# Optimization experiments

Measured on AMD Instinct MI355X. Metric: run time of the kernel, lower is better.

Reference implementation:

```python
import jax, jax.numpy as jnp
import numpy as np

VOCAB, P, K, B, L, R = 50257, 512, 64, 32, 2048, 5


def setup_inputs() -> dict:
    key = jax.random.key(0)
    k1, k2, k3, k4, k5, k6, k7 = jax.random.split(key, 7)
    return {
        "x": jax.random.randint(k1, (B, L), 0, VOCAB, dtype=jnp.int32),
        "V": jax.random.normal(k2, (VOCAB, P), dtype=jnp.float32),
        "C": jax.random.normal(k3, (K, P), dtype=jnp.float32),
        "f1_w": jax.random.normal(k4, (2 * R + 1,), dtype=jnp.float32),
        "f1_b": jax.random.normal(k5, (K,), dtype=jnp.float32),
        "f2_w": jax.random.normal(k6, (K, P), dtype=jnp.float32),
        "f2_b": jax.random.normal(k7, (K,), dtype=jnp.float32),
    }


def reference(x, V, C, f1_w, f1_b, f2_w, f2_b):
    b, l = x.shape
    k, p = C.shape
    w = f1_w.shape[0]
    r = (w - 1) // 2
    emb = V[x]                                              # [B,L,P] embedding lookup
    x_hat = emb / jnp.linalg.norm(emb, axis=2, keepdims=True)
    l_hat = C / jnp.linalg.norm(C, axis=1, keepdims=True)
    G = jnp.einsum('kp,blp->bkl', l_hat, x_hat)             # cosine sim [B,K,L]
    # sliding-window dot product == depthwise 1D cross-correlation, 'same' padding
    u = jax.lax.conv_general_dilated(
        G.reshape(b * k, 1, l), f1_w.reshape(1, 1, w),
        window_strides=(1,), padding=[(r, r)],
        dimension_numbers=('NCH', 'OIH', 'NCH'),
    ).reshape(b, k, l)
    m = jax.nn.relu(u + f1_b[None, :, None])                # [B,K,L]
    beta = jax.nn.softmax(m.max(axis=1), axis=1)            # max over labels, softmax over seq -> [B,L]
    pooled = jnp.mean(beta[:, :, None] * emb, axis=1)       # [B,P]
    return pooled @ f2_w.T + f2_b                           # [B,K]
```

## Files before the change

kernel.cpp:

```cpp
#include <hip/hip_runtime.h>
#include <hip/hip_bf16.h>

#define PP     512
#define KK     64
#define BB     32
#define LLEN   2048
#define SROWS  74

typedef __attribute__((ext_vector_type(8)))  short short8;
typedef __attribute__((ext_vector_type(16))) float float16;

__device__ inline unsigned int pack_bf2(float lo, float hi) {
    __hip_bfloat162 h = __float22bfloat162_rn(make_float2(lo, hi));
    unsigned int u;
    __builtin_memcpy(&u, &h, 4);
    return u;
}
__device__ inline float bf_lo(unsigned int v) { return __uint_as_float(v << 16); }
__device__ inline float bf_hi(unsigned int v) { return __uint_as_float(v & 0xffff0000u); }

__global__ void k1_prep(const float* __restrict__ C, const float* __restrict__ f2w,
                        ushort* __restrict__ Bu) {
    const int n = blockIdx.x;
    const float* src = (n < 64) ? (C + n * PP) : (f2w + (n - 64) * PP);
    const int t = threadIdx.x;
    float v0 = src[t];
    float v1 = src[t + 256];
    __shared__ float red[256];
    red[t] = v0 * v0 + v1 * v1;
    __syncthreads();
    for (int s = 128; s > 0; s >>= 1) {
        if (t < s) red[t] += red[t + s];
        __syncthreads();
    }
    const float inv = (n < 64) ? rsqrtf(red[0]) : 1.f;
    Bu[(((t >> 3)       * 128 + n) << 3) + (t & 7)] = (ushort)(pack_bf2(v0 * inv, 0.f) & 0xffffu);
    Bu[((((t + 256) >> 3)) * 128 + n) * 8 + (t & 7)] = (ushort)(pack_bf2(v1 * inv, 0.f) & 0xffffu);
}

__launch_bounds__(512, 4)
__global__ void k2_fused(const int* __restrict__ x, const float* __restrict__ V,
                         const uint4* __restrict__ Bu4,
                         const float* __restrict__ f1w, const float* __restrict__ f1b,
                         float* __restrict__ pool) {
    __shared__ uint4 sA[SROWS * 64];
    __shared__ int   stok[SROWS];
    __shared__ float rnorm[SROWS];
    __shared__ float smv[64];
    __shared__ float sp[64];
    __shared__ float sscal[2];

    const int tid  = threadIdx.x;
    const int lane = tid & 63;
    const int wv   = tid >> 6;
    const int l31  = lane & 31;
    const int b    = blockIdx.x >> 5;
    const int l0   = (blockIdx.x & 31) * 64;

    if (tid < SROWS) {
        int gl = l0 - 5 + tid;
        gl = min(max(gl, 0), LLEN - 1);
        stok[tid] = x[b * LLEN + gl];
    }
    __syncthreads();

    {
        const int o = tid & 7;
        const int r = tid >> 3;
        const float* src = V + (size_t)stok[r] * PP + o * 4;
        const int swzr = r & 7;
        float nrm = 0.f;
        float4 pa[8];
#pragma unroll
        for (int g = 0; g < 8; ++g) pa[g] = ((const float4*)src)[g * 8];
        float4 pb[8];
#pragma unroll
        for (int g = 0; g < 8; ++g) pb[g] = ((const float4*)src)[(g + 8) * 8];
#pragma unroll
        for (int g = 0; g < 8; ++g) {
            const float4 a = pa[g];
            nrm = fmaf(a.x, a.x, fmaf(a.y, a.y, fmaf(a.z, a.z, fmaf(a.w, a.w, nrm))));
            uint2 w2; w2.x = pack_bf2(a.x, a.y); w2.y = pack_bf2(a.z, a.w);
            const int f = g * 4 + (o >> 1);
            ((uint2*)&sA[r * 64 + (f ^ swzr)])[o & 1] = w2;
        }
#pragma unroll
        for (int g = 0; g < 8; ++g) {
            const float4 a = pb[g];
            nrm = fmaf(a.x, a.x, fmaf(a.y, a.y, fmaf(a.z, a.z, fmaf(a.w, a.w, nrm))));
            uint2 w2; w2.x = pack_bf2(a.x, a.y); w2.y = pack_bf2(a.z, a.w);
            const int f = (g + 8) * 4 + (o >> 1);
            ((uint2*)&sA[r * 64 + (f ^ swzr)])[o & 1] = w2;
        }
        nrm += __shfl_xor(nrm, 1, 64);
        nrm += __shfl_xor(nrm, 2, 64);
        nrm += __shfl_xor(nrm, 4, 64);
        if (o == 0) rnorm[r] = rsqrtf(nrm);
    }
    if (tid < 160) {
        const int h16 = tid & 15;
        const int r   = 64 + (tid >> 4);
        const float* src = V + (size_t)stok[r] * PP + h16 * 4;
        const int swzr = r & 7;
        float nrm = 0.f;
        float4 ph[8];
#pragma unroll
        for (int g = 0; g < 8; ++g) ph[g] = ((const float4*)src)[g * 16];
#pragma unroll
        for (int g = 0; g < 8; ++g) {
            const float4 a = ph[g];
            nrm = fmaf(a.x, a.x, fmaf(a.y, a.y, fmaf(a.z, a.z, fmaf(a.w, a.w, nrm))));
            uint2 w2; w2.x = pack_bf2(a.x, a.y); w2.y = pack_bf2(a.z, a.w);
            const int f = g * 8 + (h16 >> 1);
            ((uint2*)&sA[r * 64 + (f ^ swzr)])[h16 & 1] = w2;
        }
        nrm += __shfl_xor(nrm, 1, 64);
        nrm += __shfl_xor(nrm, 2, 64);
        nrm += __shfl_xor(nrm, 4, 64);
        nrm += __shfl_xor(nrm, 8, 64);
        if (h16 == 0) rnorm[r] = rsqrtf(nrm);
    }
    __syncthreads();

    float16 c0, c1;
#pragma unroll
    for (int i = 0; i < 16; ++i) { c0[i] = 0.f; c1[i] = 0.f; }

    const int rowBase = (wv == 0) ? 0 : (wv == 1) ? 32 : (wv == 2) ? 42
                      : (wv == 3) ? 5 : 37;
    const int cc = lane >> 5;
    if (wv < 5) {
        const int nh    = (wv < 3) ? 0 : 64;
        const int row   = rowBase + l31;
        const int abase = row * 64;
        const int aswz  = row & 7;
#pragma unroll 8
        for (int ks = 0; ks < 32; ++ks) {
            const int ff = ks * 2 + cc;
            const uint4 av = sA[abase + (ff ^ aswz)];
            const uint4 b0 = Bu4[ff * 128 + nh + l31];
            const uint4 b1 = Bu4[ff * 128 + nh + 32 + l31];
            short8 a8, t0, t1;
            __builtin_memcpy(&a8, &av, 16);
            __builtin_memcpy(&t0, &b0, 16);
            __builtin_memcpy(&t1, &b1, 16);
            c0 = __builtin_amdgcn_mfma_f32_32x32x16_bf16(a8, t0, c0, 0, 0, 0);
            c1 = __builtin_amdgcn_mfma_f32_32x32x16_bf16(a8, t1, c1, 0, 0, 0);
        }
    }
    __syncthreads();

    unsigned int* G32 = (unsigned int*)sA;
    float*        E2s = (float*)((char*)sA + 10240);
    float*        sred = (float*)((char*)sA + 28672);
    if (wv < 3) {
#pragma unroll
        for (int reg = 0; reg < 16; ++reg) {
            const int rr  = (reg & 3) + 8 * (reg >> 2) + 4 * cc;
            const int row = rowBase + rr;
            if (wv == 2 && row < 64) continue;
            const int gl = l0 - 5 + row;
            unsigned int vpk = 0u;
            if (gl >= 0 && gl < LLEN) {
                const float rn = rnorm[row];
                vpk = pack_bf2(c0[reg] * rn, c1[reg] * rn);
            }
            G32[row * 32 + l31] = vpk;
        }
    } else if (wv < 5) {
#pragma unroll
        for (int reg = 0; reg < 16; ++reg) {
            const int rr = (reg & 3) + 8 * (reg >> 2) + 4 * cc;
            const int o  = rowBase - 5 + rr;
            E2s[o * 64 + l31]      = c0[reg];
            E2s[o * 64 + 32 + l31] = c1[reg];
        }
    }
    __syncthreads();

    float w[11];
#pragma unroll
    for (int t = 0; t < 11; ++t) w[t] = f1w[t];
    const int j = l31;
    const int h = tid >> 5;
    const float bias0 = f1b[j], bias1 = f1b[j + 32];
#pragma unroll
    for (int i = 0; i < 4; ++i) {
        const int o = i * 16 + h;
        float u0 = 0.f, u1 = 0.f;
#pragma unroll
        for (int tap = 0; tap < 11; ++tap) {
            const unsigned int v = G32[(o + tap) * 32 + j];
            u0 = fmaf(bf_lo(v), w[tap], u0);
            u1 = fmaf(bf_hi(v), w[tap], u1);
        }
        float m = fmaxf(fmaxf(u0 + bias0, 0.f), fmaxf(u1 + bias1, 0.f));
#pragma unroll
        for (int off = 16; off > 0; off >>= 1)
            m = fmaxf(m, __shfl_xor(m, off, 64));
        if (j == 0) smv[o] = m;
    }
    __syncthreads();

    if (tid < 64) {
        float v = smv[tid];
#pragma unroll
        for (int off = 32; off > 0; off >>= 1)
            v = fmaxf(v, __shfl_xor(v, off, 64));
        if (tid == 0) sscal[0] = v;
    }
    __syncthreads();
    const float mx = sscal[0];
    if (tid < 64) sp[tid] = __expf(smv[tid] - mx);
    __syncthreads();
    if (tid < 64) {
        float s = sp[tid];
#pragma unroll
        for (int off = 32; off > 0; off >>= 1)
            s += __shfl_xor(s, off, 64);
        if (tid == 0) sscal[1] = s;
    }

    float a0 = 0.f, a1 = 0.f;
#pragma unroll
    for (int i = 0; i < 4; ++i) {
        const int o = i * 16 + h;
        const float wgt = sp[o];
        a0 = fmaf(wgt, E2s[o * 64 + j], a0);
        a1 = fmaf(wgt, E2s[o * 64 + 32 + j], a1);
    }
    __syncthreads();
    sred[h * 64 + j]      = a0;
    sred[h * 64 + j + 32] = a1;
    __syncthreads();
    if (tid < 64) {
        float r = 0.f;
#pragma unroll
        for (int hh = 0; hh < 16; ++hh) r += sred[hh * 64 + tid];
        float* dst = pool + (size_t)blockIdx.x * 68;
        dst[tid] = r;
        if (tid == 0) { dst[64] = sscal[0]; dst[65] = sscal[1]; }
    }
}

__global__ void k6_final(const float* __restrict__ pool, const float* __restrict__ f2b,
                         float* __restrict__ out) {
    const int b = blockIdx.x;
    const int k = threadIdx.x;
    float M = -1e30f;
#pragma unroll
    for (int c = 0; c < 32; ++c)
        M = fmaxf(M, pool[(size_t)(b * 32 + c) * 68 + 64]);
    float tot = 0.f, num = 0.f;
#pragma unroll
    for (int c = 0; c < 32; ++c) {
        const float* pc = pool + (size_t)(b * 32 + c) * 68;
        const float sc = __expf(pc[64] - M);
        tot = fmaf(sc, pc[65], tot);
        num = fmaf(sc, pc[k], num);
    }
    out[b * KK + k] = (num / tot) * (1.f / 2048.f) + f2b[k];
}

extern "C" void kernel_launch(void* const* d_in, const int* in_sizes, int n_in,
                              void* d_out, int out_size, void* d_ws, size_t ws_size,
                              hipStream_t stream) {
    const int*   x   = (const int*)d_in[0];
    const float* V   = (const float*)d_in[1];
    const float* C   = (const float*)d_in[2];
    const float* f1w = (const float*)d_in[3];
    const float* f1b = (const float*)d_in[4];
    const float* f2w = (const float*)d_in[5];
    const float* f2b = (const float*)d_in[6];
    float* out = (float*)d_out;

    float* ws = (float*)d_ws;
    ushort* Bu = (ushort*)ws;
    float* pool = ws + 32768;

    k1_prep <<<128, 256, 0, stream>>>(C, f2w, Bu);
    k2_fused<<<BB * 32, 512, 0, stream>>>(x, V, (const uint4*)Bu, f1w, f1b, pool);
    k6_final<<<BB, 64, 0, stream>>>(pool, f2b, out);
}
```

Before: 185.2 us.

## Halve per-block sequence tile to 32 positions and double grid size

Each fused block now handles 32 sequence positions (42 rows including halo) instead of 64 (74 rows), so the grid grows to 2048 blocks and LDS use per block shrinks. Launch bounds are raised to allow more resident blocks per CU, and the MFMA wave assignment is remapped to three waves. The halo overhead (10 extra gathered rows per 32 positions instead of per 64) increases redundant embedding loads, and more waves sit idle during the matmul. The final reduction loops over 64 chunks instead of 32.

```diff
diff --git a/kernel.cpp b/kernel.cpp
--- a/kernel.cpp
+++ b/kernel.cpp
@@ -5,7 +5,9 @@
 #define KK     64
 #define BB     32
 #define LLEN   2048
-#define SROWS  74
+#define TPOS   32
+#define SROWS  42
+#define NCHUNK (LLEN / TPOS)
 
 typedef __attribute__((ext_vector_type(8)))  short short8;
 typedef __attribute__((ext_vector_type(16))) float float16;
@@ -38,7 +40,7 @@
     Bu[((((t + 256) >> 3)) * 128 + n) * 8 + (t & 7)] = (ushort)(pack_bf2(v1 * inv, 0.f) & 0xffffu);
 }
 
-__launch_bounds__(512, 4)
+__launch_bounds__(512, 6)
 __global__ void k2_fused(const int* __restrict__ x, const float* __restrict__ V,
                          const uint4* __restrict__ Bu4,
                          const float* __restrict__ f1w, const float* __restrict__ f1b,
@@ -46,16 +48,16 @@
     __shared__ uint4 sA[SROWS * 64];
     __shared__ int   stok[SROWS];
     __shared__ float rnorm[SROWS];
-    __shared__ float smv[64];
-    __shared__ float sp[64];
+    __shared__ float smv[TPOS];
+    __shared__ float sp[TPOS];
     __shared__ float sscal[2];
 
     const int tid  = threadIdx.x;
     const int lane = tid & 63;
     const int wv   = tid >> 6;
     const int l31  = lane & 31;
-    const int b    = blockIdx.x >> 5;
-    const int l0   = (blockIdx.x & 31) * 64;
+    const int b    = blockIdx.x >> 6;
+    const int l0   = (blockIdx.x & 63) * TPOS;
 
     if (tid < SROWS) {
         int gl = l0 - 5 + tid;
@@ -64,73 +66,53 @@
     }
     __syncthreads();
 
-    {
+    if (tid < SROWS * 8) {
         const int o = tid & 7;
         const int r = tid >> 3;
         const float* src = V + (size_t)stok[r] * PP + o * 4;
         const int swzr = r & 7;
         float nrm = 0.f;
-        float4 pa[8];
-#pragma unroll
-        for (int g = 0; g < 8; ++g) pa[g] = ((const float4*)src)[g * 8];
-        float4 pb[8];
-#pragma unroll
-        for (int g = 0; g < 8; ++g) pb[g] = ((const float4*)src)[(g + 8) * 8];
-#pragma unroll
-        for (int g = 0; g < 8; ++g) {
-            const float4 a = pa[g];
-            nrm = fmaf(a.x, a.x, fmaf(a.y, a.y, fmaf(a.z, a.z, fmaf(a.w, a.w, nrm))));
-            uint2 w2; w2.x = pack_bf2(a.x, a.y); w2.y = pack_bf2(a.z, a.w);
-            const int f = g * 4 + (o >> 1);
-            ((uint2*)&sA[r * 64 + (f ^ swzr)])[o & 1] = w2;
-        }
-#pragma unroll
-        for (int g = 0; g < 8; ++g) {
-            const float4 a = pb[g];
-            nrm = fmaf(a.x, a.x, fmaf(a.y, a.y, fmaf(a.z, a.z, fmaf(a.w, a.w, nrm))));
-            uint2 w2; w2.x = pack_bf2(a.x, a.y); w2.y = pack_bf2(a.z, a.w);
-            const int f = (g + 8) * 4 + (o >> 1);
-            ((uint2*)&sA[r * 64 + (f ^ swzr)])[o & 1] = w2;
+        {
+            float4 pa[8];
+#pragma unroll
+            for (int g = 0; g < 8; ++g) pa[g] = ((const float4*)src)[g * 8];
+#pragma unroll
+            for (int g = 0; g < 8; ++g) {
+                const float4 a = pa[g];
+                nrm = fmaf(a.x, a.x, fmaf(a.y, a.y, fmaf(a.z, a.z, fmaf(a.w, a.w, nrm))));
+                uint2 w2; w2.x = pack_bf2(a.x, a.y); w2.y = pack_bf2(a.z, a.w);
+                const int f = g * 4 + (o >> 1);
+                ((uint2*)&sA[r * 64 + (f ^ swzr)])[o & 1] = w2;
+            }
+        }
+        {
+            float4 pb[8];
+#pragma unroll
+            for (int g = 0; g < 8; ++g) pb[g] = ((const float4*)src)[(g + 8) * 8];
+#pragma unroll
+            for (int g = 0; g < 8; ++g) {
+                const float4 a = pb[g];
+                nrm = fmaf(a.x, a.x, fmaf(a.y, a.y, fmaf(a.z, a.z, fmaf(a.w, a.w, nrm))));
+                uint2 w2; w2.x = pack_bf2(a.x, a.y); w2.y = pack_bf2(a.z, a.w);
+                const int f = (g + 8) * 4 + (o >> 1);
+                ((uint2*)&sA[r * 64 + (f ^ swzr)])[o & 1] = w2;
+            }
         }
         nrm += __shfl_xor(nrm, 1, 64);
         nrm += __shfl_xor(nrm, 2, 64);
         nrm += __shfl_xor(nrm, 4, 64);
         if (o == 0) rnorm[r] = rsqrtf(nrm);
     }
-    if (tid < 160) {
-        const int h16 = tid & 15;
-        const int r   = 64 + (tid >> 4);
-        const float* src = V + (size_t)stok[r] * PP + h16 * 4;
-        const int swzr = r & 7;
-        float nrm = 0.f;
-        float4 ph[8];
-#pragma unroll
-        for (int g = 0; g < 8; ++g) ph[g] = ((const float4*)src)[g * 16];
-#pragma unroll
-        for (int g = 0; g < 8; ++g) {
-            const float4 a = ph[g];
-            nrm = fmaf(a.x, a.x, fmaf(a.y, a.y, fmaf(a.z, a.z, fmaf(a.w, a.w, nrm))));
-            uint2 w2; w2.x = pack_bf2(a.x, a.y); w2.y = pack_bf2(a.z, a.w);
-            const int f = g * 8 + (h16 >> 1);
-            ((uint2*)&sA[r * 64 + (f ^ swzr)])[h16 & 1] = w2;
-        }
-        nrm += __shfl_xor(nrm, 1, 64);
-        nrm += __shfl_xor(nrm, 2, 64);
-        nrm += __shfl_xor(nrm, 4, 64);
-        nrm += __shfl_xor(nrm, 8, 64);
-        if (h16 == 0) rnorm[r] = rsqrtf(nrm);
-    }
     __syncthreads();
 
     float16 c0, c1;
 #pragma unroll
     for (int i = 0; i < 16; ++i) { c0[i] = 0.f; c1[i] = 0.f; }
 
-    const int rowBase = (wv == 0) ? 0 : (wv == 1) ? 32 : (wv == 2) ? 42
-                      : (wv == 3) ? 5 : 37;
+    const int rowBase = (wv == 0) ? 0 : (wv == 1) ? 10 : 5;
     const int cc = lane >> 5;
-    if (wv < 5) {
-        const int nh    = (wv < 3) ? 0 : 64;
+    if (wv < 3) {
+        const int nh    = (wv < 2) ? 0 : 64;
         const int row   = rowBase + l31;
         const int abase = row * 64;
         const int aswz  = row & 7;
@@ -151,14 +133,14 @@
     __syncthreads();
 
     unsigned int* G32 = (unsigned int*)sA;
-    float*        E2s = (float*)((char*)sA + 10240);
-    float*        sred = (float*)((char*)sA + 28672);
-    if (wv < 3) {
+    float*        E2s = (float*)((char*)sA + 5632);
+    float*        sred = (float*)((char*)sA + 14336);
+    if (wv < 2) {
 #pragma unroll
         for (int reg = 0; reg < 16; ++reg) {
             const int rr  = (reg & 3) + 8 * (reg >> 2) + 4 * cc;
             const int row = rowBase + rr;
-            if (wv == 2 && row < 64) continue;
+            if (wv == 1 && row < 32) continue;
             const int gl = l0 - 5 + row;
             unsigned int vpk = 0u;
             if (gl >= 0 && gl < LLEN) {
@@ -167,11 +149,11 @@
             }
             G32[row * 32 + l31] = vpk;
         }
-    } else if (wv < 5) {
+    } else if (wv == 2) {
 #pragma unroll
         for (int reg = 0; reg < 16; ++reg) {
             const int rr = (reg & 3) + 8 * (reg >> 2) + 4 * cc;
-            const int o  = rowBase - 5 + rr;
+            const int o  = rr;
             E2s[o * 64 + l31]      = c0[reg];
             E2s[o * 64 + 32 + l31] = c1[reg];
         }
@@ -185,7 +167,7 @@
     const int h = tid >> 5;
     const float bias0 = f1b[j], bias1 = f1b[j + 32];
 #pragma unroll
-    for (int i = 0; i < 4; ++i) {
+    for (int i = 0; i < 2; ++i) {
         const int o = i * 16 + h;
         float u0 = 0.f, u1 = 0.f;
 #pragma unroll
@@ -202,28 +184,28 @@
     }
     __syncthreads();
 
-    if (tid < 64) {
+    if (tid < 32) {
         float v = smv[tid];
 #pragma unroll
-        for (int off = 32; off > 0; off >>= 1)
+        for (int off = 16; off > 0; off >>= 1)
             v = fmaxf(v, __shfl_xor(v, off, 64));
         if (tid == 0) sscal[0] = v;
     }
     __syncthreads();
     const float mx = sscal[0];
-    if (tid < 64) sp[tid] = __expf(smv[tid] - mx);
-    __syncthreads();
-    if (tid < 64) {
+    if (tid < 32) sp[tid] = __expf(smv[tid] - mx);
+    __syncthreads();
+    if (tid < 32) {
         float s = sp[tid];
 #pragma unroll
-        for (int off = 32; off > 0; off >>= 1)
+        for (int off = 16; off > 0; off >>= 1)
             s += __shfl_xor(s, off, 64);
         if (tid == 0) sscal[1] = s;
     }
 
     float a0 = 0.f, a1 = 0.f;
 #pragma unroll
-    for (int i = 0; i < 4; ++i) {
+    for (int i = 0; i < 2; ++i) {
         const int o = i * 16 + h;
         const float wgt = sp[o];
         a0 = fmaf(wgt, E2s[o * 64 + j], a0);
@@ -248,13 +230,13 @@
     const int b = blockIdx.x;
     const int k = threadIdx.x;
     float M = -1e30f;
-#pragma unroll
-    for (int c = 0; c < 32; ++c)
-        M = fmaxf(M, pool[(size_t)(b * 32 + c) * 68 + 64]);
+#pragma unroll 8
+    for (int c = 0; c < NCHUNK; ++c)
+        M = fmaxf(M, pool[(size_t)(b * NCHUNK + c) * 68 + 64]);
     float tot = 0.f, num = 0.f;
-#pragma unroll
-    for (int c = 0; c < 32; ++c) {
-        const float* pc = pool + (size_t)(b * 32 + c) * 68;
+#pragma unroll 8
+    for (int c = 0; c < NCHUNK; ++c) {
+        const float* pc = pool + (size_t)(b * NCHUNK + c) * 68;
         const float sc = __expf(pc[64] - M);
         tot = fmaf(sc, pc[65], tot);
         num = fmaf(sc, pc[k], num);
@@ -279,6 +261,6 @@
     float* pool = ws + 32768;
 
     k1_prep <<<128, 256, 0, stream>>>(C, f2w, Bu);
-    k2_fused<<<BB * 32, 512, 0, stream>>>(x, V, (const uint4*)Bu, f1w, f1b, pool);
+    k2_fused<<<BB * NCHUNK, 512, 0, stream>>>(x, V, (const uint4*)Bu, f1w, f1b, pool);
     k6_final<<<BB, 64, 0, stream>>>(pool, f2b, out);
 }
```

Measured after the change: 207.7 us. 1.12x slower.

## Make fused kernel persistent over four chunks with double-buffered embedding prefetch

Applied to the files above, without the earlier changes.

Each block now handles four consecutive 64-position chunks instead of one. Shared staging buffers are doubled so the next chunk's token ids and embedding-row loads go out before the current chunk's MFMA, and the packing happens after it, overlapping gather latency with compute. The grid shrinks to a quarter, which means fewer blocks across the CUs (256 blocks for roughly 256 CUs). Launch bounds are relaxed to two blocks per SM to make room for the extra prefetch registers, at the cost of lower occupancy.

```diff
diff --git a/kernel.cpp b/kernel.cpp
--- a/kernel.cpp
+++ b/kernel.cpp
@@ -5,7 +5,10 @@
 #define KK     64
 #define BB     32
 #define LLEN   2048
+#define TPOS   64
 #define SROWS  74
+#define NCHUNK (LLEN / TPOS)
+#define CPB    4
 
 typedef __attribute__((ext_vector_type(8)))  short short8;
 typedef __attribute__((ext_vector_type(16))) float float16;
@@ -38,51 +41,73 @@
     Bu[((((t + 256) >> 3)) * 128 + n) * 8 + (t & 7)] = (ushort)(pack_bf2(v1 * inv, 0.f) & 0xffffu);
 }
 
-__launch_bounds__(512, 4)
+__launch_bounds__(512, 2)
 __global__ void k2_fused(const int* __restrict__ x, const float* __restrict__ V,
                          const uint4* __restrict__ Bu4,
                          const float* __restrict__ f1w, const float* __restrict__ f1b,
                          float* __restrict__ pool) {
-    __shared__ uint4 sA[SROWS * 64];
-    __shared__ int   stok[SROWS];
-    __shared__ float rnorm[SROWS];
-    __shared__ float smv[64];
-    __shared__ float sp[64];
+    __shared__ uint4 sA[2][SROWS * 64];
+    __shared__ int   stok[2][SROWS];
+    __shared__ float rnorm[2][SROWS];
+    __shared__ float smv[TPOS];
+    __shared__ float sp[TPOS];
     __shared__ float sscal[2];
 
     const int tid  = threadIdx.x;
     const int lane = tid & 63;
     const int wv   = tid >> 6;
     const int l31  = lane & 31;
-    const int b    = blockIdx.x >> 5;
-    const int l0   = (blockIdx.x & 31) * 64;
-
-    if (tid < SROWS) {
-        int gl = l0 - 5 + tid;
-        gl = min(max(gl, 0), LLEN - 1);
-        stok[tid] = x[b * LLEN + gl];
-    }
-    __syncthreads();
-
-    {
-        const int o = tid & 7;
-        const int r = tid >> 3;
-        const float* src = V + (size_t)stok[r] * PP + o * 4;
+    const int chunk0 = blockIdx.x * CPB;
+
+    const int o   = tid & 7;
+    const int r   = tid >> 3;
+    const int ht  = tid - 352;
+    const int h16 = ht & 15;
+    const int rh  = 64 + (ht >> 4);
+
+    float4 pa[8], pb[8], ph[8];
+
+    const int rowBase = (wv == 0) ? 0 : (wv == 1) ? 32 : (wv == 2) ? 42
+                      : (wv == 3) ? 5 : 37;
+    const int cc = lane >> 5;
+
+    float w[11];
+#pragma unroll
+    for (int t = 0; t < 11; ++t) w[t] = f1w[t];
+    const int j = l31;
+    const int h = tid >> 5;
+    const float bias0 = f1b[j], bias1 = f1b[j + 32];
+
+    auto LOADTOK = [&](int bi, int chunk) {
+        if (tid < SROWS) {
+            const int bb = chunk >> 5;
+            const int l0 = (chunk & 31) * TPOS;
+            int gl = min(max(l0 - 5 + tid, 0), LLEN - 1);
+            stok[bi][tid] = x[bb * LLEN + gl];
+        }
+    };
+    auto ISSUE = [&](int bi) {
+        const float4* f4 = (const float4*)(V + (size_t)stok[bi][r] * PP);
+#pragma unroll
+        for (int g = 0; g < 8; ++g) pa[g] = f4[o + g * 8];
+#pragma unroll
+        for (int g = 0; g < 8; ++g) pb[g] = f4[o + (g + 8) * 8];
+        if (ht >= 0) {
+            const float4* f4h = (const float4*)(V + (size_t)stok[bi][rh] * PP);
+#pragma unroll
+            for (int g = 0; g < 8; ++g) ph[g] = f4h[h16 + g * 16];
+        }
+    };
+    auto PACK = [&](int bi) {
         const int swzr = r & 7;
         float nrm = 0.f;
-        float4 pa[8];
-#pragma unroll
-        for (int g = 0; g < 8; ++g) pa[g] = ((const float4*)src)[g * 8];
-        float4 pb[8];
-#pragma unroll
-        for (int g = 0; g < 8; ++g) pb[g] = ((const float4*)src)[(g + 8) * 8];
 #pragma unroll
         for (int g = 0; g < 8; ++g) {
             const float4 a = pa[g];
             nrm = fmaf(a.x, a.x, fmaf(a.y, a.y, fmaf(a.z, a.z, fmaf(a.w, a.w, nrm))));
             uint2 w2; w2.x = pack_bf2(a.x, a.y); w2.y = pack_bf2(a.z, a.w);
             const int f = g * 4 + (o >> 1);
-            ((uint2*)&sA[r * 64 + (f ^ swzr)])[o & 1] = w2;
+            ((uint2*)&sA[bi][r * 64 + (f ^ swzr)])[o & 1] = w2;
         }
 #pragma unroll
         for (int g = 0; g < 8; ++g) {
@@ -90,156 +115,163 @@
             nrm = fmaf(a.x, a.x, fmaf(a.y, a.y, fmaf(a.z, a.z, fmaf(a.w, a.w, nrm))));
             uint2 w2; w2.x = pack_bf2(a.x, a.y); w2.y = pack_bf2(a.z, a.w);
             const int f = (g + 8) * 4 + (o >> 1);
-            ((uint2*)&sA[r * 64 + (f ^ swzr)])[o & 1] = w2;
+            ((uint2*)&sA[bi][r * 64 + (f ^ swzr)])[o & 1] = w2;
         }
         nrm += __shfl_xor(nrm, 1, 64);
         nrm += __shfl_xor(nrm, 2, 64);
         nrm += __shfl_xor(nrm, 4, 64);
-        if (o == 0) rnorm[r] = rsqrtf(nrm);
-    }
-    if (tid < 160) {
-        const int h16 = tid & 15;
-        const int r   = 64 + (tid >> 4);
-        const float* src = V + (size_t)stok[r] * PP + h16 * 4;
-        const int swzr = r & 7;
-        float nrm = 0.f;
-        float4 ph[8];
-#pragma unroll
-        for (int g = 0; g < 8; ++g) ph[g] = ((const float4*)src)[g * 16];
-#pragma unroll
-        for (int g = 0; g < 8; ++g) {
-            const float4 a = ph[g];
-            nrm = fmaf(a.x, a.x, fmaf(a.y, a.y, fmaf(a.z, a.z, fmaf(a.w, a.w, nrm))));
-            uint2 w2; w2.x = pack_bf2(a.x, a.y); w2.y = pack_bf2(a.z, a.w);
-            const int f = g * 8 + (h16 >> 1);
-            ((uint2*)&sA[r * 64 + (f ^ swzr)])[h16 & 1] = w2;
-        }
-        nrm += __shfl_xor(nrm, 1, 64);
-        nrm += __shfl_xor(nrm, 2, 64);
-        nrm += __shfl_xor(nrm, 4, 64);
-        nrm += __shfl_xor(nrm, 8, 64);
-        if (h16 == 0) rnorm[r] = rsqrtf(nrm);
-    }
+        if (o == 0) rnorm[bi][r] = rsqrtf(nrm);
+        if (ht >= 0) {
+            const int swzh = rh & 7;
+            float nh2 = 0.f;
+#pragma unroll
+            for (int g = 0; g < 8; ++g) {
+                const float4 a = ph[g];
+                nh2 = fmaf(a.x, a.x, fmaf(a.y, a.y, fmaf(a.z, a.z, fmaf(a.w, a.w, nh2))));
+                uint2 w2; w2.x = pack_bf2(a.x, a.y); w2.y = pack_bf2(a.z, a.w);
+                const int f = g * 8 + (h16 >> 1);
+                ((uint2*)&sA[bi][rh * 64 + (f ^ swzh)])[h16 & 1] = w2;
+            }
+            nh2 += __shfl_xor(nh2, 1, 64);
+            nh2 += __shfl_xor(nh2, 2, 64);
+            nh2 += __shfl_xor(nh2, 4, 64);
+            nh2 += __shfl_xor(nh2, 8, 64);
+            if (h16 == 0) rnorm[bi][rh] = rsqrtf(nh2);
+        }
+    };
+
+    int cur = 0;
+    LOADTOK(0, chunk0);
     __syncthreads();
-
-    float16 c0, c1;
-#pragma unroll
-    for (int i = 0; i < 16; ++i) { c0[i] = 0.f; c1[i] = 0.f; }
-
-    const int rowBase = (wv == 0) ? 0 : (wv == 1) ? 32 : (wv == 2) ? 42
-                      : (wv == 3) ? 5 : 37;
-    const int cc = lane >> 5;
-    if (wv < 5) {
-        const int nh    = (wv < 3) ? 0 : 64;
-        const int row   = rowBase + l31;
-        const int abase = row * 64;
-        const int aswz  = row & 7;
+    ISSUE(0);
+    PACK(0);
+
+#pragma unroll 1
+    for (int i = 0; i < CPB; ++i) {
+        const int chunk = chunk0 + i;
+        const int l0 = (chunk & 31) * TPOS;
+        const int nxt = cur ^ 1;
+
+        if (i + 1 < CPB) LOADTOK(nxt, chunk + 1);
+        __syncthreads();
+
+        if (i + 1 < CPB) ISSUE(nxt);
+        __builtin_amdgcn_sched_barrier(0);
+
+        float16 c0, c1;
+#pragma unroll
+        for (int k = 0; k < 16; ++k) { c0[k] = 0.f; c1[k] = 0.f; }
+        if (wv < 5) {
+            const int nh    = (wv < 3) ? 0 : 64;
+            const int row   = rowBase + l31;
+            const int abase = row * 64;
+            const int aswz  = row & 7;
 #pragma unroll 8
-        for (int ks = 0; ks < 32; ++ks) {
-            const int ff = ks * 2 + cc;
-            const uint4 av = sA[abase + (ff ^ aswz)];
-            const uint4 b0 = Bu4[ff * 128 + nh + l31];
-            const uint4 b1 = Bu4[ff * 128 + nh + 32 + l31];
-            short8 a8, t0, t1;
-            __builtin_memcpy(&a8, &av, 16);
-            __builtin_memcpy(&t0, &b0, 16);
-            __builtin_memcpy(&t1, &b1, 16);
-            c0 = __builtin_amdgcn_mfma_f32_32x32x16_bf16(a8, t0, c0, 0, 0, 0);
-            c1 = __builtin_amdgcn_mfma_f32_32x32x16_bf16(a8, t1, c1, 0, 0, 0);
-        }
-    }
-    __syncthreads();
-
-    unsigned int* G32 = (unsigned int*)sA;
-    float*        E2s = (float*)((char*)sA + 10240);
-    float*        sred = (float*)((char*)sA + 28672);
-    if (wv < 3) {
-#pragma unroll
-        for (int reg = 0; reg < 16; ++reg) {
-            const int rr  = (reg & 3) + 8 * (reg >> 2) + 4 * cc;
-            const int row = rowBase + rr;
-            if (wv == 2 && row < 64) continue;
-            const int gl = l0 - 5 + row;
-            unsigned int vpk = 0u;
-            if (gl >= 0 && gl < LLEN) {
-                const float rn = rnorm[row];
-                vpk = pack_bf2(c0[reg] * rn, c1[reg] * rn);
-            }
-            G32[row * 32 + l31] = vpk;
-        }
-    } else if (wv < 5) {
-#pragma unroll
-        for (int reg = 0; reg < 16; ++reg) {
-            const int rr = (reg & 3) + 8 * (reg >> 2) + 4 * cc;
-            const int o  = rowBase - 5 + rr;
-            E2s[o * 64 + l31]      = c0[reg];
-            E2s[o * 64 + 32 + l31] = c1[reg];
-        }
-    }
-    __syncthreads();
-
-    float w[11];
-#pragma unroll
-    for (int t = 0; t < 11; ++t) w[t] = f1w[t];
-    const int j = l31;
-    const int h = tid >> 5;
-    const float bias0 = f1b[j], bias1 = f1b[j + 32];
-#pragma unroll
-    for (int i = 0; i < 4; ++i) {
-        const int o = i * 16 + h;
-        float u0 = 0.f, u1 = 0.f;
-#pragma unroll
-        for (int tap = 0; tap < 11; ++tap) {
-            const unsigned int v = G32[(o + tap) * 32 + j];
-            u0 = fmaf(bf_lo(v), w[tap], u0);
-            u1 = fmaf(bf_hi(v), w[tap], u1);
-        }
-        float m = fmaxf(fmaxf(u0 + bias0, 0.f), fmaxf(u1 + bias1, 0.f));
-#pragma unroll
-        for (int off = 16; off > 0; off >>= 1)
-            m = fmaxf(m, __shfl_xor(m, off, 64));
-        if (j == 0) smv[o] = m;
-    }
-    __syncthreads();
-
-    if (tid < 64) {
-        float v = smv[tid];
-#pragma unroll
-        for (int off = 32; off > 0; off >>= 1)
-            v = fmaxf(v, __shfl_xor(v, off, 64));
-        if (tid == 0) sscal[0] = v;
-    }
-    __syncthreads();
-    const float mx = sscal[0];
-    if (tid < 64) sp[tid] = __expf(smv[tid] - mx);
-    __syncthreads();
-    if (tid < 64) {
-        float s = sp[tid];
-#pragma unroll
-        for (int off = 32; off > 0; off >>= 1)
-            s += __shfl_xor(s, off, 64);
-        if (tid == 0) sscal[1] = s;
-    }
-
-    float a0 = 0.f, a1 = 0.f;
-#pragma unroll
-    for (int i = 0; i < 4; ++i) {
-        const int o = i * 16 + h;
-        const float wgt = sp[o];
-        a0 = fmaf(wgt, E2s[o * 64 + j], a0);
-        a1 = fmaf(wgt, E2s[o * 64 + 32 + j], a1);
-    }
-    __syncthreads();
-    sred[h * 64 + j]      = a0;
-    sred[h * 64 + j + 32] = a1;
-    __syncthreads();
-    if (tid < 64) {
-        float r = 0.f;
-#pragma unroll
-        for (int hh = 0; hh < 16; ++hh) r += sred[hh * 64 + tid];
-        float* dst = pool + (size_t)blockIdx.x * 68;
-        dst[tid] = r;
-        if (tid == 0) { dst[64] = sscal[0]; dst[65] = sscal[1]; }
+            for (int ks = 0; ks < 32; ++ks) {
+                const int ff = ks * 2 + cc;
+                const uint4 av = sA[cur][abase + (ff ^ aswz)];
+                const uint4 b0 = Bu4[ff * 128 + nh + l31];
+                const uint4 b1 = Bu4[ff * 128 + nh + 32 + l31];
+                short8 a8, t0, t1;
+                __builtin_memcpy(&a8, &av, 16);
+                __builtin_memcpy(&t0, &b0, 16);
+                __builtin_memcpy(&t1, &b1, 16);
+                c0 = __builtin_amdgcn_mfma_f32_32x32x16_bf16(a8, t0, c0, 0, 0, 0);
+                c1 = __builtin_amdgcn_mfma_f32_32x32x16_bf16(a8, t1, c1, 0, 0, 0);
+            }
+        }
+        __builtin_amdgcn_sched_barrier(0);
+        __syncthreads();
+
+        if (i + 1 < CPB) PACK(nxt);
+
+        unsigned int* G32 = (unsigned int*)&sA[cur][0];
+        float*        E2s = (float*)((char*)&sA[cur][0] + 10240);
+        float*        sred = (float*)((char*)&sA[cur][0] + 28672);
+        if (wv < 3) {
+#pragma unroll
+            for (int reg = 0; reg < 16; ++reg) {
+                const int rr  = (reg & 3) + 8 * (reg >> 2) + 4 * cc;
+                const int row = rowBase + rr;
+                if (wv == 2 && row < 64) continue;
+                const int gl = l0 - 5 + row;
+                unsigned int vpk = 0u;
+                if (gl >= 0 && gl < LLEN) {
+                    const float rn = rnorm[cur][row];
+                    vpk = pack_bf2(c0[reg] * rn, c1[reg] * rn);
+                }
+                G32[row * 32 + l31] = vpk;
+            }
+        } else if (wv < 5) {
+#pragma unroll
+            for (int reg = 0; reg < 16; ++reg) {
+                const int rr = (reg & 3) + 8 * (reg >> 2) + 4 * cc;
+                const int oo = rowBase - 5 + rr;
+                E2s[oo * 64 + l31]      = c0[reg];
+                E2s[oo * 64 + 32 + l31] = c1[reg];
+            }
+        }
+        __syncthreads();
+
+#pragma unroll
+        for (int it = 0; it < 4; ++it) {
+            const int oo = it * 16 + h;
+            float u0 = 0.f, u1 = 0.f;
+#pragma unroll
+            for (int tap = 0; tap < 11; ++tap) {
+                const unsigned int v = G32[(oo + tap) * 32 + j];
+                u0 = fmaf(bf_lo(v), w[tap], u0);
+                u1 = fmaf(bf_hi(v), w[tap], u1);
+            }
+            float m = fmaxf(fmaxf(u0 + bias0, 0.f), fmaxf(u1 + bias1, 0.f));
+#pragma unroll
+            for (int off = 16; off > 0; off >>= 1)
+                m = fmaxf(m, __shfl_xor(m, off, 64));
+            if (j == 0) smv[oo] = m;
+        }
+        __syncthreads();
+
+        if (tid < 64) {
+            float v = smv[tid];
+#pragma unroll
+            for (int off = 32; off > 0; off >>= 1)
+                v = fmaxf(v, __shfl_xor(v, off, 64));
+            if (tid == 0) sscal[0] = v;
+        }
+        __syncthreads();
+        const float mx = sscal[0];
+        if (tid < 64) sp[tid] = __expf(smv[tid] - mx);
+        __syncthreads();
+        if (tid < 64) {
+            float s = sp[tid];
+#pragma unroll
+            for (int off = 32; off > 0; off >>= 1)
+                s += __shfl_xor(s, off, 64);
+            if (tid == 0) sscal[1] = s;
+        }
+
+        float a0 = 0.f, a1 = 0.f;
+#pragma unroll
+        for (int it = 0; it < 4; ++it) {
+            const int oo = it * 16 + h;
+            const float wgt = sp[oo];
+            a0 = fmaf(wgt, E2s[oo * 64 + j], a0);
+            a1 = fmaf(wgt, E2s[oo * 64 + 32 + j], a1);
+        }
+        __syncthreads();
+        sred[h * 64 + j]      = a0;
+        sred[h * 64 + j + 32] = a1;
+        __syncthreads();
+        if (tid < 64) {
+            float rr = 0.f;
+#pragma unroll
+            for (int hh = 0; hh < 16; ++hh) rr += sred[hh * 64 + tid];
+            float* dst = pool + (size_t)chunk * 68;
+            dst[tid] = rr;
+            if (tid == 0) { dst[64] = sscal[0]; dst[65] = sscal[1]; }
+        }
+        __syncthreads();
+        cur ^= 1;
     }
 }
 
@@ -249,12 +281,12 @@
     const int k = threadIdx.x;
     float M = -1e30f;
 #pragma unroll
-    for (int c = 0; c < 32; ++c)
-        M = fmaxf(M, pool[(size_t)(b * 32 + c) * 68 + 64]);
+    for (int c = 0; c < NCHUNK; ++c)
+        M = fmaxf(M, pool[(size_t)(b * NCHUNK + c) * 68 + 64]);
     float tot = 0.f, num = 0.f;
 #pragma unroll
-    for (int c = 0; c < 32; ++c) {
-        const float* pc = pool + (size_t)(b * 32 + c) * 68;
+    for (int c = 0; c < NCHUNK; ++c) {
+        const float* pc = pool + (size_t)(b * NCHUNK + c) * 68;
         const float sc = __expf(pc[64] - M);
         tot = fmaf(sc, pc[65], tot);
         num = fmaf(sc, pc[k], num);
@@ -279,6 +311,6 @@
     float* pool = ws + 32768;
 
     k1_prep <<<128, 256, 0, stream>>>(C, f2w, Bu);
-    k2_fused<<<BB * 32, 512, 0, stream>>>(x, V, (const uint4*)Bu, f1w, f1b, pool);
+    k2_fused<<<(BB * NCHUNK) / CPB, 512, 0, stream>>>(x, V, (const uint4*)Bu, f1w, f1b, pool);
     k6_final<<<BB, 64, 0, stream>>>(pool, f2b, out);
 }
```

After: 207.9 us. +12.3%, slower.
